# Kernel optimization log

Measured on AMD Instinct MI355X. Metric: run time of the kernel, lower is better.

The kernel has to match this reference:

```python
import jax, jax.numpy as jnp
import numpy as np

EMB = 1024
NH = 16
HS = EMB // NH

def setup_inputs() -> dict:
    key = jax.random.key(0)
    ks = jax.random.split(key, 9)
    s = 0.02
    x = jax.random.normal(ks[0], (4, 2048, EMB), dtype=jnp.float32)
    Wq = jax.random.normal(ks[1], (EMB, EMB), dtype=jnp.float32) * s
    bq = jnp.zeros((EMB,), jnp.float32)
    Wk = jax.random.normal(ks[2], (EMB, EMB), dtype=jnp.float32) * s
    bk = jnp.zeros((EMB,), jnp.float32)
    Wv = jax.random.normal(ks[3], (EMB, EMB), dtype=jnp.float32) * s
    bv = jnp.zeros((EMB,), jnp.float32)
    Wo = jax.random.normal(ks[4], (EMB, EMB), dtype=jnp.float32) * s
    bo = jnp.zeros((EMB,), jnp.float32)
    return {"x": x, "Wq": Wq, "bq": bq, "Wk": Wk, "bk": bk,
            "Wv": Wv, "bv": bv, "Wo": Wo, "bo": bo}

def reference(x, Wq, bq, Wk, bk, Wv, bv, Wo, bo):
    B, T, C = x.shape
    q = x @ Wq + bq
    k = x @ Wk + bk
    v = x @ Wv + bv
    # [B, H, T, hs]
    q = q.reshape(B, T, NH, HS).transpose(0, 2, 1, 3)
    k = k.reshape(B, T, NH, HS).transpose(0, 2, 1, 3)
    v = v.reshape(B, T, NH, HS).transpose(0, 2, 1, 3)
    scale = 1.0 / np.sqrt(HS).astype(np.float32)
    att = jnp.einsum('bhqd,bhkd->bhqk', q, k) * scale
    causal = jnp.tril(jnp.ones((T, T), dtype=bool))
    att = jnp.where(causal[None, None], att, jnp.float32(-jnp.inf))
    att = jax.nn.softmax(att, axis=-1)
    y = jnp.einsum('bhqk,bhkd->bhqd', att, v)
    y = y.transpose(0, 2, 1, 3).reshape(B, T, C)
    return y @ Wo + bo
```

## Files before the change

kernel.cpp:

```cpp
#include <hip/hip_runtime.h>

#define EMB   1024
#define NHEAD 16
#define HS    64
#define BATCH 4
#define SEQ   2048
#define MTOK  (BATCH*SEQ)

typedef __bf16 bf16;
typedef __bf16 bf16x8 __attribute__((ext_vector_type(8)));
typedef __bf16 bf16x4 __attribute__((ext_vector_type(4)));
typedef float  f32x4  __attribute__((ext_vector_type(4)));
typedef _Float16 f16;
typedef f16 f16x4 __attribute__((ext_vector_type(4)));
typedef f16 f16x8 __attribute__((ext_vector_type(8)));

#define MFMA16(a,b,c)     __builtin_amdgcn_mfma_f32_16x16x32_bf16(a,b,c,0,0,0)
#define MFMA_H32(a,b,c)   __builtin_amdgcn_mfma_f32_16x16x32_f16(a,b,c,0,0,0)
#define MFMA_H16(a,b,c)   __builtin_amdgcn_mfma_f32_16x16x16f16(a,b,c,0,0,0)

#if __has_builtin(__builtin_amdgcn_exp2f)
#define EXP2(x) __builtin_amdgcn_exp2f(x)
#else
#define EXP2(x) exp2f(x)
#endif

#define GLL(g, l) __builtin_amdgcn_global_load_lds(                         \
        (const __attribute__((address_space(1))) void*)(g),                 \
        (__attribute__((address_space(3))) void*)(l), 16, 0, 0)

__global__ __launch_bounds__(256) void k_prep(
        const float* __restrict__ x, bf16* __restrict__ xb,
        const float* __restrict__ W0, const float* __restrict__ W1,
        const float* __restrict__ W2, const float* __restrict__ W3,
        bf16* __restrict__ T0, bf16* __restrict__ T1,
        bf16* __restrict__ T2, bf16* __restrict__ T3) {
    const int z = blockIdx.z;
    if (z == 0) {
        const int blk = blockIdx.y * 16 + blockIdx.x;
        const size_t base = (size_t)blk * 32768;
        for (int j = threadIdx.x; j < 8192; j += 256) {
            size_t i = base + (size_t)j * 4;
            float4 v = *(const float4*)(x + i);
            bf16x4 o;
            o[0] = (bf16)v.x; o[1] = (bf16)v.y; o[2] = (bf16)v.z; o[3] = (bf16)v.w;
            *(bf16x4*)(xb + i) = o;
        }
        return;
    }
    __shared__ float tile[64][65];
    const float* W = (z == 1) ? W0 : (z == 2) ? W1 : (z == 3) ? W2 : W3;
    bf16* Wt = (z == 1) ? T0 : (z == 2) ? T1 : (z == 3) ? T2 : T3;
    int c0 = blockIdx.x * 64, r0 = blockIdx.y * 64;
    int tx = threadIdx.x & 63, ty = threadIdx.x >> 6;
    #pragma unroll
    for (int r = ty; r < 64; r += 4)
        tile[r][tx] = W[(r0 + r) * EMB + c0 + tx];
    __syncthreads();
    #pragma unroll
    for (int cc = ty; cc < 64; cc += 4)
        Wt[(c0 + cc) * EMB + r0 + tx] = (bf16)tile[tx][cc];
}

__global__ __launch_bounds__(256) void k_qkv_gemm(
        const bf16* __restrict__ xb,
        const bf16* __restrict__ Wqt, const bf16* __restrict__ Wkt, const bf16* __restrict__ Wvt,
        const float* __restrict__ bq, const float* __restrict__ bk, const float* __restrict__ bv,
        f16* __restrict__ Q, f16* __restrict__ K, f16* __restrict__ Vt) {
    __shared__ __align__(16) bf16 As[128 * 64];
    __shared__ __align__(16) bf16 Bs[128 * 64];
    const int tid = threadIdx.x;
    const int lane = tid & 63;
    const int wave = tid >> 6;
    const int l15 = lane & 15, quad = lane >> 4;
    const int wm = (wave >> 1) * 64, wn = (wave & 1) * 64;
    const int m0 = blockIdx.x * 128;
    const int gy = blockIdx.y;
    const int which = gy >> 3;
    const int n0 = (gy & 7) * 128;
    const bf16* Wt  = (which == 0) ? Wqt : (which == 1) ? Wkt : Wvt;
    const float* bias = (which == 0) ? bq : (which == 1) ? bk : bv;

    f32x4 acc[4][4];
    #pragma unroll
    for (int i = 0; i < 4; i++)
        #pragma unroll
        for (int j = 0; j < 4; j++) acc[i][j] = (f32x4){0.f, 0.f, 0.f, 0.f};

    const int r0_ = tid >> 3;
    const int kcs = ((tid & 7) ^ (r0_ & 7)) * 8;
    const bf16* Ag = xb + (size_t)m0 * EMB + r0_ * EMB + kcs;
    const bf16* Bg = Wt + (size_t)n0 * EMB + r0_ * EMB + kcs;
    const int rsw = l15 & 7;

    for (int k0 = 0; k0 < EMB; k0 += 64) {
        __syncthreads();
        #pragma unroll
        for (int g = 0; g < 4; g++) {
            GLL(Ag + 32 * g * EMB + k0, As + (tid + g * 256) * 8);
            GLL(Bg + 32 * g * EMB + k0, Bs + (tid + g * 256) * 8);
        }
        __syncthreads();

        bf16x8 af[2][4], bfr[2][4];
        #pragma unroll
        for (int h = 0; h < 2; h++) {
            #pragma unroll
            for (int rf = 0; rf < 4; rf++)
                af[h][rf] = *(const bf16x8*)(As + (wm + rf * 16 + l15) * 64 +
                                             (((4 * h + quad) ^ rsw) * 8));
            #pragma unroll
            for (int cf = 0; cf < 4; cf++)
                bfr[h][cf] = *(const bf16x8*)(Bs + (wn + cf * 16 + l15) * 64 +
                                              (((4 * h + quad) ^ rsw) * 8));
        }
        #pragma unroll
        for (int h = 0; h < 2; h++)
            #pragma unroll
            for (int rf = 0; rf < 4; rf++)
                #pragma unroll
                for (int cf = 0; cf < 4; cf++)
                    acc[rf][cf] = MFMA16(af[h][rf], bfr[h][cf], acc[rf][cf]);
    }

    const float QSCALE = 0.18033688011112043f;
    #pragma unroll
    for (int cf = 0; cf < 4; cf++) {
        const int col = n0 + wn + cf * 16 + l15;
        const float bv_ = bias[col];
        const int h = col >> 6, d = col & 63;
        #pragma unroll
        for (int rf = 0; rf < 4; rf++) {
            #pragma unroll
            for (int r = 0; r < 4; r++) {
                const int row = m0 + wm + rf * 16 + quad * 4 + r;
                const int b_ = row >> 11, t = row & (SEQ - 1);
                const float val = acc[rf][cf][r] + bv_;
                if (which == 0) {
                    Q[((size_t)(b_ * NHEAD + h) * SEQ + t) * HS + d] = (f16)(val * QSCALE);
                } else if (which == 1) {
                    K[((size_t)(b_ * NHEAD + h) * SEQ + t) * HS + d] = (f16)val;
                } else {
                    Vt[(((size_t)(b_ * NHEAD + h) * 32 + (t >> 6)) * 64 + d) * 64 + (t & 63)] = (f16)val;
                }
            }
        }
    }
}

__global__ __launch_bounds__(256) void k_attn(
        const f16* __restrict__ Q, const f16* __restrict__ K,
        const f16* __restrict__ Vt, bf16* __restrict__ y) {
    __shared__ __align__(16) f16 kbuf[2][64 * 64];
    __shared__ __align__(16) f16 vbuf[2][64 * 64];
    const int tid = threadIdx.x;
    const int wave = tid >> 6, lane = tid & 63;
    const int l15 = lane & 15, quad = lane >> 4;
    const int qtA = blockIdx.x;
    const int bh = blockIdx.y;
    const int h = bh & (NHEAD - 1), b_ = bh >> 4;

    const f16* Qb = Q + (size_t)bh * SEQ * HS;
    const f16* Kb = K + (size_t)bh * SEQ * HS;
    const f16* Vb = Vt + (size_t)bh * 32 * 4096;

    const int c0 = tid, c1 = tid + 256;
    const int soff0 = (c0 >> 3) * 64 + (((c0 & 7) ^ ((c0 >> 3) & 7)) * 8);
    const int soff1 = (c1 >> 3) * 64 + (((c1 & 7) ^ ((c1 >> 3) & 7)) * 8);
    const int swz = l15 & 7;

    f16x4 ones;
    #pragma unroll
    for (int i = 0; i < 4; i++) ones[i] = (f16)1.0f;

    #pragma unroll 1
    for (int phase = 0; phase < 2; ++phase) {
        const int qt = phase ? (15 - qtA) : qtA;
        const int ntiles = 2 * qt + 2;
        const int qrow0 = qt * 128 + wave * 32;

        f16x8 qb[2][2];
        #pragma unroll
        for (int qf = 0; qf < 2; qf++)
            #pragma unroll
            for (int dk = 0; dk < 2; dk++)
                qb[qf][dk] = *(const f16x8*)(Qb + (qrow0 + 16 * qf + l15) * HS + 32 * dk + quad * 8);

        f32x4 o[2][4], lacc[2];
        #pragma unroll
        for (int qf = 0; qf < 2; qf++) {
            lacc[qf] = (f32x4){0.f, 0.f, 0.f, 0.f};
            #pragma unroll
            for (int df = 0; df < 4; df++) o[qf][df] = (f32x4){0.f, 0.f, 0.f, 0.f};
        }

        f16x8 kr0 = *(const f16x8*)(Kb + c0 * 8);
        f16x8 kr1 = *(const f16x8*)(Kb + c1 * 8);
        f16x8 vr0 = *(const f16x8*)(Vb + c0 * 8);
        f16x8 vr1 = *(const f16x8*)(Vb + c1 * 8);
        __syncthreads();
        *(f16x8*)(kbuf[0] + soff0) = kr0;
        *(f16x8*)(kbuf[0] + soff1) = kr1;
        *(f16x8*)(vbuf[0] + soff0) = vr0;
        *(f16x8*)(vbuf[0] + soff1) = vr1;

        for (int it = 0; it < ntiles; ++it) {
            const int kv0 = it * 64;
            __syncthreads();
            if (it + 1 < ntiles) {
                const f16* kg = Kb + (size_t)(kv0 + 64) * HS;
                const f16* vg = Vb + (size_t)(it + 1) * 4096;
                kr0 = *(const f16x8*)(kg + c0 * 8);
                kr1 = *(const f16x8*)(kg + c1 * 8);
                vr0 = *(const f16x8*)(vg + c0 * 8);
                vr1 = *(const f16x8*)(vg + c1 * 8);
            }
            if (kv0 <= qrow0 + 31) {
                const f16* kb_ = kbuf[it & 1];
                const f16* vb_ = vbuf[it & 1];

                f32x4 s[4][2];
                #pragma unroll
                for (int mb = 0; mb < 4; mb++) {
                    f16x8 ka0 = *(const f16x8*)(kb_ + (16 * mb + l15) * 64 + ((quad ^ swz) * 8));
                    f16x8 ka1 = *(const f16x8*)(kb_ + (16 * mb + l15) * 64 + (((4 + quad) ^ swz) * 8));
                    #pragma unroll
                    for (int qf = 0; qf < 2; qf++) {
                        f32x4 t = (f32x4){0.f, 0.f, 0.f, 0.f};
                        t = MFMA_H32(ka0, qb[qf][0], t);
                        t = MFMA_H32(ka1, qb[qf][1], t);
                        s[mb][qf] = t;
                    }
                }

                f16x4 pa[4][2];
                const bool edge = (kv0 + 63 > qrow0);
                #pragma unroll
                for (int mb = 0; mb < 4; mb++)
                    #pragma unroll
                    for (int qf = 0; qf < 2; qf++) {
                        f16x4 p;
                        if (edge) {
                            #pragma unroll
                            for (int r = 0; r < 4; r++) {
                                const int kvc = kv0 + 16 * mb + quad * 4 + r;
                                const int qq  = qrow0 + 16 * qf + l15;
                                p[r] = (f16)((kvc <= qq) ? EXP2(s[mb][qf][r]) : 0.f);
                            }
                        } else {
                            #pragma unroll
                            for (int r = 0; r < 4; r++)
                                p[r] = (f16)EXP2(s[mb][qf][r]);
                        }
                        pa[mb][qf] = p;
                    }

                #pragma unroll
                for (int df = 0; df < 4; df++)
                    #pragma unroll
                    for (int kb = 0; kb < 4; kb++) {
                        f16x4 vfrag = *(const f16x4*)(vb_ + (16 * df + l15) * 64 +
                                        (((2 * kb + (quad >> 1)) ^ swz) * 8) + (quad & 1) * 4);
                        #pragma unroll
                        for (int qf = 0; qf < 2; qf++)
                            o[qf][df] = MFMA_H16(pa[kb][qf], vfrag, o[qf][df]);
                    }
                #pragma unroll
                for (int kb = 0; kb < 4; kb++)
                    #pragma unroll
                    for (int qf = 0; qf < 2; qf++)
                        lacc[qf] = MFMA_H16(pa[kb][qf], ones, lacc[qf]);
            }
            if (it + 1 < ntiles) {
                const int nb = (it + 1) & 1;
                *(f16x8*)(kbuf[nb] + soff0) = kr0;
                *(f16x8*)(kbuf[nb] + soff1) = kr1;
                *(f16x8*)(vbuf[nb] + soff0) = vr0;
                *(f16x8*)(vbuf[nb] + soff1) = vr1;
            }
        }

        #pragma unroll
        for (int qf = 0; qf < 2; qf++)
            #pragma unroll
            for (int r = 0; r < 4; r++) {
                float inv = 1.f / lacc[qf][r];
                int t = qrow0 + 16 * qf + quad * 4 + r;
                bf16* yp = y + ((size_t)(b_ * SEQ + t)) * EMB + h * HS;
                #pragma unroll
                for (int df = 0; df < 4; df++)
                    yp[df * 16 + l15] = (bf16)(o[qf][df][r] * inv);
            }
    }
}

__global__ __launch_bounds__(256) void k_out_gemm(
        const bf16* __restrict__ y, const bf16* __restrict__ Wot,
        const float* __restrict__ bo, float* __restrict__ out) {
    __shared__ __align__(16) bf16 As[128 * 64];
    __shared__ __align__(16) bf16 Bs[128 * 64];
    const int tid = threadIdx.x;
    const int lane = tid & 63;
    const int wave = tid >> 6;
    const int l15 = lane & 15, quad = lane >> 4;
    const int wm = (wave >> 1) * 64, wn = (wave & 1) * 64;
    const int m0 = blockIdx.x * 128;
    const int n0 = blockIdx.y * 128;

    f32x4 acc[4][4];
    #pragma unroll
    for (int i = 0; i < 4; i++)
        #pragma unroll
        for (int j = 0; j < 4; j++) acc[i][j] = (f32x4){0.f, 0.f, 0.f, 0.f};

    const int r0_ = tid >> 3;
    const int kcs = ((tid & 7) ^ (r0_ & 7)) * 8;
    const bf16* Ag = y   + (size_t)m0 * EMB + r0_ * EMB + kcs;
    const bf16* Bg = Wot + (size_t)n0 * EMB + r0_ * EMB + kcs;
    const int rsw = l15 & 7;

    for (int k0 = 0; k0 < EMB; k0 += 64) {
        __syncthreads();
        #pragma unroll
        for (int g = 0; g < 4; g++) {
            GLL(Ag + 32 * g * EMB + k0, As + (tid + g * 256) * 8);
            GLL(Bg + 32 * g * EMB + k0, Bs + (tid + g * 256) * 8);
        }
        __syncthreads();

        bf16x8 af[2][4], bfr[2][4];
        #pragma unroll
        for (int h = 0; h < 2; h++) {
            #pragma unroll
            for (int rf = 0; rf < 4; rf++)
                af[h][rf] = *(const bf16x8*)(As + (wm + rf * 16 + l15) * 64 +
                                             (((4 * h + quad) ^ rsw) * 8));
            #pragma unroll
            for (int cf = 0; cf < 4; cf++)
                bfr[h][cf] = *(const bf16x8*)(Bs + (wn + cf * 16 + l15) * 64 +
                                              (((4 * h + quad) ^ rsw) * 8));
        }
        #pragma unroll
        for (int h = 0; h < 2; h++)
            #pragma unroll
            for (int rf = 0; rf < 4; rf++)
                #pragma unroll
                for (int cf = 0; cf < 4; cf++)
                    acc[rf][cf] = MFMA16(af[h][rf], bfr[h][cf], acc[rf][cf]);
    }

    #pragma unroll
    for (int cf = 0; cf < 4; cf++) {
        const int col = n0 + wn + cf * 16 + l15;
        const float bv_ = bo[col];
        #pragma unroll
        for (int rf = 0; rf < 4; rf++) {
            #pragma unroll
            for (int r = 0; r < 4; r++) {
                const int row = m0 + wm + rf * 16 + quad * 4 + r;
                out[(size_t)row * EMB + col] = acc[rf][cf][r] + bv_;
            }
        }
    }
}

extern "C" void kernel_launch(void* const* d_in, const int* in_sizes, int n_in,
                              void* d_out, int out_size, void* d_ws, size_t ws_size,
                              hipStream_t stream) {
    const float* x  = (const float*)d_in[0];
    const float* Wq = (const float*)d_in[1];
    const float* bq = (const float*)d_in[2];
    const float* Wk = (const float*)d_in[3];
    const float* bk = (const float*)d_in[4];
    const float* Wv = (const float*)d_in[5];
    const float* bv = (const float*)d_in[6];
    const float* Wo = (const float*)d_in[7];
    const float* bo = (const float*)d_in[8];
    float* out = (float*)d_out;

    char* ws = (char*)d_ws;
    bf16* xb  = (bf16*)(ws);
    bf16* Wqt = (bf16*)(ws + (16u << 20));
    bf16* Wkt = (bf16*)(ws + (18u << 20));
    bf16* Wvt = (bf16*)(ws + (20u << 20));
    bf16* Wot = (bf16*)(ws + (22u << 20));
    f16*  Q   = (f16*)(ws + (24u << 20));
    f16*  K   = (f16*)(ws + (40u << 20));
    f16*  Vt  = (f16*)(ws + (56u << 20));
    bf16* y   = (bf16*)(ws + (72u << 20));

    dim3 gp(16, 16, 5);
    k_prep<<<gp, 256, 0, stream>>>(x, xb, Wq, Wk, Wv, Wo, Wqt, Wkt, Wvt, Wot);

    dim3 g1(MTOK / 128, 24);
    k_qkv_gemm<<<g1, 256, 0, stream>>>(xb, Wqt, Wkt, Wvt, bq, bk, bv, Q, K, Vt);

    dim3 g2(SEQ / 256, BATCH * NHEAD);
    k_attn<<<g2, 256, 0, stream>>>(Q, K, Vt, y);

    dim3 g3(MTOK / 128, EMB / 128);
    k_out_gemm<<<g3, 256, 0, stream>>>(y, Wot, bo, out);
}
```

Before: 286.7 us.

## Rewrite QKV GEMM with 256x256 tiles, 4-stage async LDS pipeline and block swizzle

```diff
diff --git a/kernel.cpp b/kernel.cpp
--- a/kernel.cpp
+++ b/kernel.cpp
@@ -62,86 +62,114 @@
         Wt[(c0 + cc) * EMB + r0 + tx] = (bf16)tile[tx][cc];
 }
 
-__global__ __launch_bounds__(256) void k_qkv_gemm(
+__global__ __launch_bounds__(512, 2) void k_qkv_gemm(
         const bf16* __restrict__ xb,
         const bf16* __restrict__ Wqt, const bf16* __restrict__ Wkt, const bf16* __restrict__ Wvt,
         const float* __restrict__ bq, const float* __restrict__ bk, const float* __restrict__ bv,
         f16* __restrict__ Q, f16* __restrict__ K, f16* __restrict__ Vt) {
-    __shared__ __align__(16) bf16 As[128 * 64];
-    __shared__ __align__(16) bf16 Bs[128 * 64];
+    __shared__ __align__(16) bf16 As[4][8192];
+    __shared__ __align__(16) bf16 Bs[4][8192];
     const int tid = threadIdx.x;
     const int lane = tid & 63;
     const int wave = tid >> 6;
     const int l15 = lane & 15, quad = lane >> 4;
-    const int wm = (wave >> 1) * 64, wn = (wave & 1) * 64;
-    const int m0 = blockIdx.x * 128;
-    const int gy = blockIdx.y;
-    const int which = gy >> 3;
-    const int n0 = (gy & 7) * 128;
-    const bf16* Wt  = (which == 0) ? Wqt : (which == 1) ? Wkt : Wvt;
+    const int wm = wave >> 2;
+    const int wn = wave & 3;
+
+    const int bid = blockIdx.x;
+    const int swz = (bid & 7) * 48 + (bid >> 3);
+    const int mt = swz & 31;
+    const int nt = swz >> 5;
+    const int which = nt >> 2;
+    const int n0 = (nt & 3) * 256;
+
+    const bf16* Wt   = (which == 0) ? Wqt : (which == 1) ? Wkt : Wvt;
     const float* bias = (which == 0) ? bq : (which == 1) ? bk : bv;
 
-    f32x4 acc[4][4];
-    #pragma unroll
-    for (int i = 0; i < 4; i++)
+    f32x4 acc[8][4];
+    #pragma unroll
+    for (int i = 0; i < 8; i++)
         #pragma unroll
         for (int j = 0; j < 4; j++) acc[i][j] = (f32x4){0.f, 0.f, 0.f, 0.f};
 
-    const int r0_ = tid >> 3;
-    const int kcs = ((tid & 7) ^ (r0_ & 7)) * 8;
-    const bf16* Ag = xb + (size_t)m0 * EMB + r0_ * EMB + kcs;
-    const bf16* Bg = Wt + (size_t)n0 * EMB + r0_ * EMB + kcs;
-    const int rsw = l15 & 7;
-
-    for (int k0 = 0; k0 < EMB; k0 += 64) {
-        __syncthreads();
-        #pragma unroll
-        for (int g = 0; g < 4; g++) {
-            GLL(Ag + 32 * g * EMB + k0, As + (tid + g * 256) * 8);
-            GLL(Bg + 32 * g * EMB + k0, Bs + (tid + g * 256) * 8);
-        }
-        __syncthreads();
-
-        bf16x8 af[2][4], bfr[2][4];
-        #pragma unroll
-        for (int h = 0; h < 2; h++) {
-            #pragma unroll
-            for (int rf = 0; rf < 4; rf++)
-                af[h][rf] = *(const bf16x8*)(As + (wm + rf * 16 + l15) * 64 +
-                                             (((4 * h + quad) ^ rsw) * 8));
-            #pragma unroll
-            for (int cf = 0; cf < 4; cf++)
-                bfr[h][cf] = *(const bf16x8*)(Bs + (wn + cf * 16 + l15) * 64 +
-                                              (((4 * h + quad) ^ rsw) * 8));
-        }
-        #pragma unroll
-        for (int h = 0; h < 2; h++)
-            #pragma unroll
-            for (int rf = 0; rf < 4; rf++)
-                #pragma unroll
-                for (int cf = 0; cf < 4; cf++)
-                    acc[rf][cf] = MFMA16(af[h][rf], bfr[h][cf], acc[rf][cf]);
-    }
+    const int P  = tid >> 3, s8 = tid & 7;
+    const int c  = s8 ^ (P & 7);
+    const int r_ = 2 * P + (c >> 2);
+    const int kc = c & 3;
+    const bf16* Asrc = xb + (size_t)(mt * 256 + r_) * EMB + kc * 8;
+    const bf16* Bsrc = Wt + (size_t)(n0 + r_) * EMB + kc * 8;
+
+#define QSTAGE(t, q) do {                                                   \
+        GLL(Asrc + (t) * 32,                 &As[q][tid * 8]);              \
+        GLL(Asrc + 128 * EMB + (t) * 32,     &As[q][tid * 8 + 4096]);       \
+        GLL(Bsrc + (t) * 32,                 &Bs[q][tid * 8]);              \
+        GLL(Bsrc + 128 * EMB + (t) * 32,     &Bs[q][tid * 8 + 4096]); } while (0)
+
+    int aoff[8], boff[4];
+    #pragma unroll
+    for (int mf = 0; mf < 8; mf++) {
+        int row = wm * 128 + mf * 16 + l15;
+        int p = row >> 1;
+        int slot = (((row & 1) << 2) | quad) ^ (p & 7);
+        aoff[mf] = p * 64 + slot * 8;
+    }
+    #pragma unroll
+    for (int nf = 0; nf < 4; nf++) {
+        int row = wn * 64 + nf * 16 + l15;
+        int p = row >> 1;
+        int slot = (((row & 1) << 2) | quad) ^ (p & 7);
+        boff[nf] = p * 64 + slot * 8;
+    }
+
+    QSTAGE(0, 0);
+    QSTAGE(1, 1);
+
+    #pragma unroll
+    for (int t = 0; t < 32; t++) {
+        if (t < 31) asm volatile("s_waitcnt vmcnt(4)" ::: "memory");
+        else        asm volatile("s_waitcnt vmcnt(0)" ::: "memory");
+        __builtin_amdgcn_s_barrier();
+        asm volatile("" ::: "memory");
+
+        const bf16* Ab = As[t & 3];
+        const bf16* Bb = Bs[t & 3];
+        bf16x8 a[8], b[4];
+        #pragma unroll
+        for (int mf = 0; mf < 8; mf++) a[mf] = *(const bf16x8*)(Ab + aoff[mf]);
+        #pragma unroll
+        for (int nf = 0; nf < 4; nf++) b[nf] = *(const bf16x8*)(Bb + boff[nf]);
+
+        if (t + 2 < 32) QSTAGE(t + 2, (t + 2) & 3);
+
+        __builtin_amdgcn_s_setprio(1);
+        #pragma unroll
+        for (int mf = 0; mf < 8; mf++)
+            #pragma unroll
+            for (int nf = 0; nf < 4; nf++)
+                acc[mf][nf] = MFMA16(a[mf], b[nf], acc[mf][nf]);
+        __builtin_amdgcn_s_setprio(0);
+    }
+#undef QSTAGE
 
     const float QSCALE = 0.18033688011112043f;
     #pragma unroll
-    for (int cf = 0; cf < 4; cf++) {
-        const int col = n0 + wn + cf * 16 + l15;
+    for (int nf = 0; nf < 4; nf++) {
+        const int col = n0 + wn * 64 + nf * 16 + l15;
         const float bv_ = bias[col];
         const int h = col >> 6, d = col & 63;
         #pragma unroll
-        for (int rf = 0; rf < 4; rf++) {
+        for (int mf = 0; mf < 8; mf++) {
             #pragma unroll
             for (int r = 0; r < 4; r++) {
-                const int row = m0 + wm + rf * 16 + quad * 4 + r;
-                const int b_ = row >> 11, t = row & (SEQ - 1);
-                const float val = acc[rf][cf][r] + bv_;
+                const int row = mt * 256 + wm * 128 + mf * 16 + quad * 4 + r;
+                const int b_ = row >> 11, tk = row & (SEQ - 1);
+                const float val = acc[mf][nf][r] + bv_;
                 if (which == 0) {
-                    Q[((size_t)(b_ * NHEAD + h) * SEQ + t) * HS + d] = (f16)(val * QSCALE);
+                    Q[((size_t)(b_ * NHEAD + h) * SEQ + tk) * HS + d] = (f16)(val * QSCALE);
                 } else if (which == 1) {
-                    K[((size_t)(b_ * NHEAD + h) * SEQ + t) * HS + d] = (f16)val;
+                    K[((size_t)(b_ * NHEAD + h) * SEQ + tk) * HS + d] = (f16)val;
                 } else {
-                    Vt[(((size_t)(b_ * NHEAD + h) * 32 + (t >> 6)) * 64 + d) * 64 + (t & 63)] = (f16)val;
+                    Vt[(((size_t)(b_ * NHEAD + h) * 32 + (tk >> 6)) * 64 + d) * 64 + (tk & 63)] = (f16)val;
                 }
             }
         }
@@ -392,8 +420,8 @@
     dim3 gp(16, 16, 5);
     k_prep<<<gp, 256, 0, stream>>>(x, xb, Wq, Wk, Wv, Wo, Wqt, Wkt, Wvt, Wot);
 
-    dim3 g1(MTOK / 128, 24);
-    k_qkv_gemm<<<g1, 256, 0, stream>>>(xb, Wqt, Wkt, Wvt, bq, bk, bv, Q, K, Vt);
+    dim3 g1(384);
+    k_qkv_gemm<<<g1, 512, 0, stream>>>(xb, Wqt, Wkt, Wvt, bq, bk, bv, Q, K, Vt);
 
     dim3 g2(SEQ / 256, BATCH * NHEAD);
     k_attn<<<g2, 256, 0, stream>>>(Q, K, Vt, y);
```

Measured after the change: 322.9 us. 12.6% more time.
